# Kernel tuning notes

Measured on AMD Instinct MI355X. Metric: run time of the kernel, lower is better.

Reference implementation:

```python
import jax, jax.numpy as jnp
import numpy as np

D = 1024
H = 16
HD = D // H  # 64
HIDDEN = ((int(D * 8 / 3) + 63) // 64) * 64  # 2752
EPS = 1e-6


def rmsnorm(x, w):
    rms = jnp.sqrt(jnp.mean(x * x, axis=-1, keepdims=True) + EPS)
    return x / rms * w


def setup_inputs() -> dict:
    key = jax.random.key(0)
    ks = jax.random.split(key, 12)
    s = lambda fan_in: 1.0 / np.sqrt(fan_in)
    return {
        "x": jax.random.normal(ks[0], (4, 16, 256, D), dtype=jnp.float32),
        "time_emb": jax.random.normal(ks[1], (4, D), dtype=jnp.float32),
        "norm1_w": jnp.ones((D,), dtype=jnp.float32),
        "norm2_w": jnp.ones((D,), dtype=jnp.float32),
        # weights stored (in, out), i.e. transpose of torch nn.Linear.weight
        "qkv_w": jax.random.normal(ks[2], (D, 3 * H * HD), dtype=jnp.float32) * s(D),
        "out_w": jax.random.normal(ks[3], (H * HD, D), dtype=jnp.float32) * s(H * HD),
        "w1": jax.random.normal(ks[4], (D, HIDDEN), dtype=jnp.float32) * s(D),
        "w2": jax.random.normal(ks[5], (D, HIDDEN), dtype=jnp.float32) * s(D),
        "w3": jax.random.normal(ks[6], (HIDDEN, D), dtype=jnp.float32) * s(HIDDEN),
        "mod_w": jax.random.normal(ks[7], (D, 6 * D), dtype=jnp.float32) * s(D),
        "mod_b": jnp.zeros((6 * D,), dtype=jnp.float32),
    }


def spatial_attention(h, qkv_w, out_w):
    # h: (B, T, S, D); attention over S independently per (B, T)
    B, T, S, _ = h.shape
    qkv = jnp.einsum('btsd,de->btse', h, qkv_w)  # (B,T,S,3*H*HD)
    qkv = qkv.reshape(B, T, S, 3, H, HD)
    q, k, v = qkv[..., 0, :, :], qkv[..., 1, :, :], qkv[..., 2, :, :]  # (B,T,S,H,HD)
    scale = HD ** -0.5
    scores = jnp.einsum('btqhd,btkhd->bthqk', q, k) * scale  # (B,T,H,S,S)
    attn = jax.nn.softmax(scores, axis=-1)
    out = jnp.einsum('bthqk,btkhd->btqhd', attn, v).reshape(B, T, S, H * HD)
    return jnp.einsum('btse,ed->btsd', out, out_w)


def reference(x, time_emb, norm1_w, norm2_w, qkv_w, out_w, w1, w2, w3, mod_w, mod_b):
    # adaLN modulation from (B, D) time_emb -> broadcast over (T, S)
    mod = jax.nn.silu(time_emb) @ mod_w + mod_b  # (B, 6D)
    mod = mod[:, None, None, :]  # (B,1,1,6D)
    shift1, scale1, gate1, shift2, scale2, gate2 = jnp.split(mod, 6, axis=-1)

    h = rmsnorm(x, norm1_w) * (1.0 + scale1) + shift1
    h = spatial_attention(h, qkv_w, out_w)
    x = x + gate1 * h

    h = rmsnorm(x, norm2_w) * (1.0 + scale2) + shift2
    h = (jax.nn.silu(h @ w1) * (h @ w2)) @ w3  # SwiGLU
    x = x + gate2 * h
    return x
```

## Files before the change

kernel.cpp:

```cpp
#include <hip/hip_runtime.h>
#include <stdint.h>


using bf16x8 = __attribute__((ext_vector_type(8))) short;
using f32x4  = __attribute__((ext_vector_type(4))) float;

typedef __attribute__((address_space(3))) uint16_t lds16_t;

__device__ __forceinline__ float bf2f(uint16_t h) {
  union { uint32_t u; float f; } v; v.u = ((uint32_t)h) << 16; return v.f;
}
__device__ __forceinline__ uint16_t f2bf(float f) {
  union { float f; uint32_t u; } v; v.f = f;
  uint32_t r = v.u + 0x7FFFu + ((v.u >> 16) & 1u);
  return (uint16_t)(r >> 16);
}
__device__ __forceinline__ float silu(float x) { return x / (1.0f + __expf(-x)); }

__device__ __forceinline__ void gload16(const uint16_t* g, lds16_t* l) {
  __builtin_amdgcn_global_load_lds(
      (const __attribute__((address_space(1))) void*)g,
      (__attribute__((address_space(3))) void*)l, 16, 0, 0);
}

__device__ __forceinline__ bf16x8 lds_rd_b128(const uint16_t* p) {
  bf16x8 r;
  uint32_t a = (uint32_t)(uintptr_t)(const lds16_t*)p;
  asm volatile("ds_read_b128 %0, %1" : "=v"(r) : "v"(a) : "memory");
  return r;
}

__global__ __launch_bounds__(256)
void transpose_cast(const float* __restrict__ w, uint16_t* __restrict__ wt,
                    int K, int N, int ldt) {
  __shared__ float tile[32][33];
  int n0 = blockIdx.x * 32, k0 = blockIdx.y * 32;
  int tx = threadIdx.x & 31, ty = threadIdx.x >> 5;
#pragma unroll
  for (int it = 0; it < 4; ++it) {
    int r = ty + it * 8;
    tile[r][tx] = w[(size_t)(k0 + r) * N + n0 + tx];
  }
  __syncthreads();
#pragma unroll
  for (int it = 0; it < 4; ++it) {
    int r = ty + it * 8;
    wt[(size_t)(n0 + r) * ldt + k0 + tx] = f2bf(tile[tx][r]);
  }
}

__global__ __launch_bounds__(1024)
void mod_kernel(const float* __restrict__ te, const float* __restrict__ mw,
                const float* __restrict__ mb, float* __restrict__ mod) {
  __shared__ float ste[4096];
  __shared__ float red[4][4][256];
  int tid = threadIdx.x;
  for (int i = tid; i < 4096; i += 1024) { float v = te[i]; ste[i] = silu(v); }
  __syncthreads();
  int kslice = tid >> 8, cl = tid & 255;
  int col = blockIdx.x * 256 + cl;
  float acc[4] = {0.f, 0.f, 0.f, 0.f};
  for (int kk = 0; kk < 256; ++kk) {
    int k = kslice * 256 + kk;
    float wv = mw[k * 6144 + col];
#pragma unroll
    for (int b = 0; b < 4; ++b) acc[b] += ste[b * 1024 + k] * wv;
  }
#pragma unroll
  for (int b = 0; b < 4; ++b) red[kslice][b][cl] = acc[b];
  __syncthreads();
  if (kslice == 0) {
#pragma unroll
    for (int b = 0; b < 4; ++b)
      mod[b * 6144 + col] =
          red[0][b][cl] + red[1][b][cl] + red[2][b][cl] + red[3][b][cl] + mb[col];
  }
}

__global__ __launch_bounds__(256)
void norm_kernel(const float* __restrict__ xf,
                 const float* __restrict__ w, const float* __restrict__ mod,
                 int shift_off, int scale_off, uint16_t* __restrict__ out) {
  int row = blockIdx.x;
  int b = row >> 12;
  int tid = threadIdx.x;
  float4 t = *(const float4*)(xf + (size_t)row * 1024 + tid * 4);
  float v[4] = {t.x, t.y, t.z, t.w};
  float ss = v[0] * v[0] + v[1] * v[1] + v[2] * v[2] + v[3] * v[3];
#pragma unroll
  for (int off = 1; off < 64; off <<= 1) ss += __shfl_xor(ss, off);
  __shared__ float red[4];
  if ((tid & 63) == 0) red[tid >> 6] = ss;
  __syncthreads();
  float tot = red[0] + red[1] + red[2] + red[3];
  float rinv = rsqrtf(tot * (1.0f / 1024.0f) + 1e-6f);
  const float* mrow = mod + b * 6144;
  uint16_t o[4];
#pragma unroll
  for (int c = 0; c < 4; ++c) {
    int col = tid * 4 + c;
    float hv = v[c] * rinv * w[col] * (1.0f + mrow[scale_off + col]) + mrow[shift_off + col];
    o[c] = f2bf(hv);
  }
  uint2 pk;
  pk.x = (uint32_t)o[0] | ((uint32_t)o[1] << 16);
  pk.y = (uint32_t)o[2] | ((uint32_t)o[3] << 16);
  *(uint2*)(out + (size_t)row * 1024 + tid * 4) = pk;
}

#define BAR __builtin_amdgcn_s_barrier()
#define LGKM0                                            \
  do {                                                   \
    asm volatile("s_waitcnt lgkmcnt(0)" ::: "memory");   \
    __builtin_amdgcn_sched_barrier(0);                   \
  } while (0)
#define VMW(N) asm volatile("s_waitcnt vmcnt(" #N ")" ::: "memory")

#define GRD4(DST, BASE, ROWB, SWZ)                                           \
  {                                                                          \
    _Pragma("unroll") for (int q_ = 0; q_ < 4; ++q_)                         \
        DST[q_] = lds_rd_b128((BASE) + ((ROWB) + q_ * 16 + col) * 64 +       \
                              (SWZ));                                        \
  }

#define MM16(I0, AF)                                                         \
  {                                                                          \
    __builtin_amdgcn_s_setprio(1);                                           \
    _Pragma("unroll") for (int q_ = 0; q_ < 4; ++q_) {                       \
      _Pragma("unroll") for (int j_ = 0; j_ < 4; ++j_)                       \
          acc[(I0) + q_][j_] = __builtin_amdgcn_mfma_f32_16x16x32_bf16(      \
              AF[q_], bf[j_], acc[(I0) + q_][j_], 0, 0, 0);                  \
    }                                                                        \
    __builtin_amdgcn_s_setprio(0);                                           \
  }

#define ADST(S, H, G) ((lds16_t*)As[(S)] + (H) * 8192 + (G) * 4096 + sdoff)
#define BDST(S, H, G) ((lds16_t*)Bs[(S)] + (H) * 8192 + (G) * 4096 + sdoff)

#define TILE(S, KA, KB, DO_A, DO_B, VMTAIL)                                  \
  {                                                                          \
    bf16x8 af[4], bf[4];                                                     \
                                                                \
    GRD4(af, As[S], wm * 128, swz0);                                         \
    GRD4(bf, Bs[S], wn * 64, swz0);                                          \
    if (DO_A) {                                                              \
      gload16(aS00 + (KA), ADST((S) ^ 1, 0, 0));                             \
      gload16(aS01 + (KA), ADST((S) ^ 1, 0, 1));                             \
    }                                                                        \
    BAR; LGKM0;                                                              \
    MM16(0, af);                                                             \
    BAR;                                                                     \
                                                                \
    GRD4(af, As[S], wm * 128 + 64, swz0);                                    \
    if (DO_A) {                                                              \
      gload16(aS10 + (KA), ADST((S) ^ 1, 1, 0));                             \
      gload16(aS11 + (KA), ADST((S) ^ 1, 1, 1));                             \
    }                                                                        \
    BAR; LGKM0;                                                              \
    MM16(4, af);                                                             \
    BAR;                                                                     \
                                                                \
    GRD4(af, As[S], wm * 128, swz1);                                         \
    GRD4(bf, Bs[S], wn * 64, swz1);                                          \
    BAR; LGKM0;                                                              \
    MM16(0, af);                                                             \
    BAR;                                                                     \
                                                                \
    GRD4(af, As[S], wm * 128 + 64, swz1);                                    \
    if (DO_B) {                                                              \
      gload16(bS00 + (KB), BDST(S, 0, 0));                                   \
      gload16(bS01 + (KB), BDST(S, 0, 1));                                   \
      gload16(bS10 + (KB), BDST(S, 1, 0));                                   \
      gload16(bS11 + (KB), BDST(S, 1, 1));                                   \
    }                                                                        \
    BAR; LGKM0;                                                              \
    MM16(4, af);                                                             \
    VMTAIL;                                                                  \
    BAR;                                                                     \
  }

template <int MODE>
__global__ __launch_bounds__(512)
void gemm256(const uint16_t* __restrict__ A, int lda,
             const uint16_t* __restrict__ Bt, int ldb,
             int N, int K, int ldc,
             uint16_t* __restrict__ obf, const float* __restrict__ xin,
             const float* __restrict__ mod, const uint16_t* __restrict__ h1,
             float* __restrict__ xio) {
  __shared__ uint16_t As[2][16384];
  __shared__ uint16_t Bs[2][16384];
  const int tiles_n = N >> 8;
  const int xcd = blockIdx.x & 7;
  const int bslot = blockIdx.x >> 3;
  const int tm = (bslot / tiles_n) * 8 + xcd;
  const int tn = bslot % tiles_n;
  const int m0 = tm * 256, n0 = tn * 256;
  const int tid = threadIdx.x;
  const int wave = tid >> 6, lane = tid & 63;
  const int wm = wave >> 2, wn = wave & 3;
  const int col = lane & 15, quad = lane >> 4;
  const int c7 = col & 7;
  const int swz0 = (quad ^ c7) << 3;
  const int swz1 = ((4 + quad) ^ c7) << 3;
  const int sdoff = wave * 512 + lane * 8;

  const int srl = lane >> 3;
  const int sl8 = ((lane & 7) ^ srl) << 3;
  const int rg0 = wave * 8 + srl;
  const int rg1 = 64 + wave * 8 + srl;
  const uint16_t* aS00 = A + (size_t)(m0 + rg0) * lda + sl8;
  const uint16_t* aS01 = A + (size_t)(m0 + rg1) * lda + sl8;
  const uint16_t* aS10 = A + (size_t)(m0 + 128 + rg0) * lda + sl8;
  const uint16_t* aS11 = A + (size_t)(m0 + 128 + rg1) * lda + sl8;
  const uint16_t* bS00 = Bt + (size_t)(n0 + rg0) * ldb + sl8;
  const uint16_t* bS01 = Bt + (size_t)(n0 + rg1) * ldb + sl8;
  const uint16_t* bS10 = Bt + (size_t)(n0 + 128 + rg0) * ldb + sl8;
  const uint16_t* bS11 = Bt + (size_t)(n0 + 128 + rg1) * ldb + sl8;

  f32x4 acc[8][4];
#pragma unroll
  for (int i = 0; i < 8; ++i)
#pragma unroll
    for (int j = 0; j < 4; ++j) acc[i][j] = (f32x4){0.f, 0.f, 0.f, 0.f};

  gload16(bS00, BDST(0, 0, 0)); gload16(bS01, BDST(0, 0, 1));
  gload16(bS10, BDST(0, 1, 0)); gload16(bS11, BDST(0, 1, 1));
  gload16(aS00, ADST(0, 0, 0)); gload16(aS01, ADST(0, 0, 1));
  gload16(aS10, ADST(0, 1, 0)); gload16(aS11, ADST(0, 1, 1));
  gload16(bS00 + 64, BDST(1, 0, 0)); gload16(bS01 + 64, BDST(1, 0, 1));
  gload16(bS10 + 64, BDST(1, 1, 0)); gload16(bS11 + 64, BDST(1, 1, 1));
  VMW(4);
  BAR;

  const int NT = K >> 6;
  int k0 = 0;
  for (int t = 0; t + 2 < NT; t += 2) {
    TILE(0, k0 + 64, k0 + 128, true, true, VMW(4));
    TILE(1, k0 + 128, k0 + 192, true, true, VMW(4));
    k0 += 128;
  }
  TILE(0, k0 + 64, 0, true, false, VMW(0));
  TILE(1, 0, 0, false, false, (void)0);

  __builtin_amdgcn_sched_barrier(0);

#pragma unroll
  for (int i = 0; i < 8; ++i) {
#pragma unroll
    for (int j = 0; j < 4; ++j) {
#pragma unroll
      for (int r = 0; r < 4; ++r) {
        int row = m0 + wm * 128 + i * 16 + quad * 4 + r;
        int cn = n0 + wn * 64 + j * 16 + col;
        float c = acc[i][j][r];
        if (MODE == 0) {
          obf[(size_t)row * ldc + cn] = f2bf(c);
        } else if (MODE == 1) {
          int b = row >> 12;
          size_t idx = (size_t)row * 1024 + cn;
          float g = mod[b * 6144 + 2048 + cn];
          xio[idx] = xin[idx] + g * c;
        } else {
          int b = row >> 12;
          size_t idx = (size_t)row * 1024 + cn;
          float g = mod[b * 6144 + 5120 + cn];
          xio[idx] = xio[idx] + g * c;
        }
      }
    }
  }
}

#define MMF(ACC, AF, BF)                                                     \
  {                                                                          \
    __builtin_amdgcn_s_setprio(1);                                           \
    _Pragma("unroll") for (int i_ = 0; i_ < 4; ++i_) {                       \
      _Pragma("unroll") for (int j_ = 0; j_ < 4; ++j_)                       \
          ACC[i_][j_] = __builtin_amdgcn_mfma_f32_16x16x32_bf16(             \
              AF[i_], BF[j_], ACC[i_][j_], 0, 0, 0);                         \
    }                                                                        \
    __builtin_amdgcn_s_setprio(0);                                           \
  }

#define FAD(S, H)  ((lds16_t*)As[(S)]  + (H) * 4096 + sdoff)
#define FB1D(S, H) ((lds16_t*)B1s[(S)] + (H) * 4096 + sdoff)
#define FB2D(S, H) ((lds16_t*)B2s[(S)] + (H) * 4096 + sdoff)

#define FTILE(S, KN, KB, DO_AB2, DO_B1, VMTAIL)                              \
  {                                                                          \
    bf16x8 af[4], bb[4];                                                     \
                      \
    GRD4(af, As[S], wm * 64, swz0);                                          \
    GRD4(bb, B1s[S], wn * 64, swz0);                                         \
    if (DO_AB2) {                                                            \
      gload16(aS[0] + (KN), FAD((S) ^ 1, 0));                                \
      gload16(aS[1] + (KN), FAD((S) ^ 1, 1));                                \
      gload16(b2S[0] + (KN), FB2D((S) ^ 1, 0));                              \
      gload16(b2S[1] + (KN), FB2D((S) ^ 1, 1));                              \
    }                                                                        \
    BAR; LGKM0;                                                              \
    MMF(acc1, af, bb);                                                       \
    BAR;                                                                     \
                                        \
    GRD4(bb, B2s[S], wn * 64, swz0);                                         \
    if (DO_AB2) {                                                            \
      gload16(aS[2] + (KN), FAD((S) ^ 1, 2));                                \
      gload16(aS[3] + (KN), FAD((S) ^ 1, 3));                                \
    }                                                                        \
    BAR; LGKM0;                                                              \
    MMF(acc2, af, bb);                                                       \
    BAR;                                                                     \
                                                     \
    GRD4(af, As[S], wm * 64, swz1);                                          \
    GRD4(bb, B1s[S], wn * 64, swz1);                                         \
    BAR; LGKM0;                                                              \
    MMF(acc1, af, bb);                                                       \
    BAR;                                                                     \
                                             \
    GRD4(bb, B2s[S], wn * 64, swz1);                                         \
    if (DO_B1) {                                                             \
      gload16(b1S[0] + (KB), FB1D(S, 0));                                    \
      gload16(b1S[1] + (KB), FB1D(S, 1));                                    \
    }                                                                        \
    BAR; LGKM0;                                                              \
    MMF(acc2, af, bb);                                                       \
    VMTAIL;                                                                  \
    BAR;                                                                     \
  }

__global__ __launch_bounds__(512)
void gemm_ffn(const uint16_t* __restrict__ A, const uint16_t* __restrict__ B1t,
              const uint16_t* __restrict__ B2t, uint16_t* __restrict__ outp) {
  __shared__ uint16_t As[2][16384];
  __shared__ uint16_t B1s[2][8192];
  __shared__ uint16_t B2s[2][8192];
  const int lda = 1024, ldb = 1024, ldc = 2816;
  const int tiles_n = 22;
  const int xcd = blockIdx.x & 7;
  const int bslot = blockIdx.x >> 3;
  const int tm = (bslot / tiles_n) * 8 + xcd;
  const int tn = bslot % tiles_n;
  const int m0 = tm * 256, n0 = tn * 128;
  const int tid = threadIdx.x;
  const int wave = tid >> 6, lane = tid & 63;
  const int wm = wave >> 1, wn = wave & 1;
  const int col = lane & 15, quad = lane >> 4;
  const int c7 = col & 7;
  const int swz0 = (quad ^ c7) << 3;
  const int swz1 = ((4 + quad) ^ c7) << 3;
  const int sdoff = wave * 512 + lane * 8;
  const int srl = lane >> 3;
  const int sl8 = ((lane & 7) ^ srl) << 3;
  const int rg = wave * 8 + srl;

  const uint16_t* aS[4];
#pragma unroll
  for (int h = 0; h < 4; ++h)
    aS[h] = A + (size_t)(m0 + h * 64 + rg) * lda + sl8;
  const uint16_t* b1S[2]; const uint16_t* b2S[2];
#pragma unroll
  for (int h = 0; h < 2; ++h) {
    b1S[h] = B1t + (size_t)(n0 + h * 64 + rg) * ldb + sl8;
    b2S[h] = B2t + (size_t)(n0 + h * 64 + rg) * ldb + sl8;
  }

  f32x4 acc1[4][4], acc2[4][4];
#pragma unroll
  for (int i = 0; i < 4; ++i)
#pragma unroll
    for (int j = 0; j < 4; ++j) {
      acc1[i][j] = (f32x4){0.f, 0.f, 0.f, 0.f};
      acc2[i][j] = (f32x4){0.f, 0.f, 0.f, 0.f};
    }

#pragma unroll
  for (int h = 0; h < 4; ++h) gload16(aS[h], FAD(0, h));
  gload16(b1S[0], FB1D(0, 0)); gload16(b1S[1], FB1D(0, 1));
  gload16(b2S[0], FB2D(0, 0)); gload16(b2S[1], FB2D(0, 1));
  gload16(b1S[0] + 64, FB1D(1, 0)); gload16(b1S[1] + 64, FB1D(1, 1));
  VMW(2);
  BAR;

  int k0 = 0;
  for (int t = 0; t + 2 < 16; t += 2) {
    FTILE(0, k0 + 64, k0 + 128, true, true, VMW(2));
    FTILE(1, k0 + 128, k0 + 192, true, true, VMW(2));
    k0 += 128;
  }
  FTILE(0, k0 + 64, 0, true, false, VMW(0));
  FTILE(1, 0, 0, false, false, (void)0);

  __builtin_amdgcn_sched_barrier(0);

#pragma unroll
  for (int i = 0; i < 4; ++i) {
#pragma unroll
    for (int j = 0; j < 4; ++j) {
#pragma unroll
      for (int r = 0; r < 4; ++r) {
        int row = m0 + wm * 64 + i * 16 + quad * 4 + r;
        int cn = n0 + wn * 64 + j * 16 + col;
        float c1 = acc1[i][j][r];
        float c2 = acc2[i][j][r];
        outp[(size_t)row * ldc + cn] = f2bf(silu(c1) * c2);
      }
    }
  }
}

__global__ __launch_bounds__(256)
void attn_kernel(const uint16_t* __restrict__ qkv, uint16_t* __restrict__ out) {
  __shared__ uint16_t lds[32768];
  const int tid = threadIdx.x;
  const int bid = blockIdx.x;
  const int slice = bid >> 2, qc = bid & 3;
  const int bt = slice >> 4, h = slice & 15;
  const int row0 = bt * 256;
  const int wave = tid >> 6, lane = tid & 63;
  const int col = lane & 15, quad = lane >> 4;

  {
    int kr = tid;
    const uint16_t* kp = qkv + (size_t)(row0 + kr) * 3072 + 1024 + h * 64;
    uint16_t* ks = lds + kr * 64;
#pragma unroll
    for (int kc = 0; kc < 8; ++kc) {
      uint4 v = *(const uint4*)(kp + kc * 8);
      *(uint4*)(ks + ((kc ^ (kr & 7)) << 3)) = v;
    }
  }
  {
    int p = tid & 127, dh = tid >> 7;
    const uint16_t* vp0 = qkv + (size_t)(row0 + 2 * p) * 3072 + 2048 + h * 64 + dh * 32;
    const uint16_t* vp1 = vp0 + 3072;
    uint16_t r0[32], r1[32];
#pragma unroll
    for (int i = 0; i < 4; ++i) {
      *(uint4*)(r0 + i * 8) = *(const uint4*)(vp0 + i * 8);
      *(uint4*)(r1 + i * 8) = *(const uint4*)(vp1 + i * 8);
    }
    uint32_t* vt = (uint32_t*)(lds + 16384);
    int krc = p >> 2;
#pragma unroll
    for (int i = 0; i < 32; ++i) {
      int d = dh * 32 + i;
      uint32_t val = (uint32_t)r0[i] | ((uint32_t)r1[i] << 16);
      vt[d * 128 + ((krc ^ (d & 7)) << 2) + (p & 3)] = val;
    }
  }
  __syncthreads();

  const int qrow = qc * 64 + wave * 16 + col;
  const uint16_t* qp = qkv + (size_t)(row0 + qrow) * 3072 + h * 64;
  bf16x8 aq0 = *(const bf16x8*)(qp + quad * 8);
  bf16x8 aq1 = *(const bf16x8*)(qp + 32 + quad * 8);

  f32x4 sc[16];
#pragma unroll
  for (int t = 0; t < 16; ++t) {
    int n = t * 16 + col;
    const uint16_t* kb = lds + n * 64;
    bf16x8 b0 = *(const bf16x8*)(kb + ((quad ^ (n & 7)) << 3));
    bf16x8 b1 = *(const bf16x8*)(kb + (((4 + quad) ^ (n & 7)) << 3));
    f32x4 s = (f32x4){0.f, 0.f, 0.f, 0.f};
    s = __builtin_amdgcn_mfma_f32_16x16x32_bf16(aq0, b0, s, 0, 0, 0);
    s = __builtin_amdgcn_mfma_f32_16x16x32_bf16(aq1, b1, s, 0, 0, 0);
    sc[t] = s;
  }

  const float scale = 0.125f;
  float inv[4];
#pragma unroll
  for (int i = 0; i < 4; ++i) {
    float m = -1e30f;
#pragma unroll
    for (int t = 0; t < 16; ++t) m = fmaxf(m, sc[t][i]);
    m = fmaxf(m, __shfl_xor(m, 1));
    m = fmaxf(m, __shfl_xor(m, 2));
    m = fmaxf(m, __shfl_xor(m, 4));
    m = fmaxf(m, __shfl_xor(m, 8));
    m *= scale;
    float sum = 0.f;
#pragma unroll
    for (int t = 0; t < 16; ++t) {
      float p = __expf(sc[t][i] * scale - m);
      sc[t][i] = p;
      sum += p;
    }
    sum += __shfl_xor(sum, 1);
    sum += __shfl_xor(sum, 2);
    sum += __shfl_xor(sum, 4);
    sum += __shfl_xor(sum, 8);
    inv[i] = 1.0f / sum;
  }
  __syncthreads();

  uint16_t* P = lds + wave * 4096;
#pragma unroll
  for (int t = 0; t < 16; ++t) {
    int pcb = t * 2 + (col >> 3);
#pragma unroll
    for (int i = 0; i < 4; ++i) {
      int r = quad * 4 + i;
      P[r * 256 + ((pcb ^ (r & 7)) << 3) + (col & 7)] = f2bf(sc[t][i] * inv[i]);
    }
  }

  f32x4 o[4];
#pragma unroll
  for (int nt = 0; nt < 4; ++nt) o[nt] = (f32x4){0.f, 0.f, 0.f, 0.f};
  const uint16_t* Vt = lds + 16384;
#pragma unroll
  for (int c = 0; c < 8; ++c) {
    int pc = c * 4 + quad;
    bf16x8 ap = *(const bf16x8*)(P + col * 256 + ((pc ^ (col & 7)) << 3));
#pragma unroll
    for (int nt = 0; nt < 4; ++nt) {
      int d = nt * 16 + col;
      bf16x8 bv = *(const bf16x8*)(Vt + d * 256 + ((pc ^ (d & 7)) << 3));
      o[nt] = __builtin_amdgcn_mfma_f32_16x16x32_bf16(ap, bv, o[nt], 0, 0, 0);
    }
  }

#pragma unroll
  for (int nt = 0; nt < 4; ++nt) {
#pragma unroll
    for (int r = 0; r < 4; ++r) {
      int grow = row0 + qc * 64 + wave * 16 + quad * 4 + r;
      int gcol = h * 64 + nt * 16 + col;
      out[(size_t)grow * 1024 + gcol] = f2bf(o[nt][r]);
    }
  }
}

extern "C" void kernel_launch(void* const* d_in, const int* in_sizes, int n_in,
                              void* d_out, int out_size, void* d_ws, size_t ws_size,
                              hipStream_t stream) {
  const float* x        = (const float*)d_in[0];
  const float* time_emb = (const float*)d_in[1];
  const float* norm1_w  = (const float*)d_in[2];
  const float* norm2_w  = (const float*)d_in[3];
  const float* qkv_w    = (const float*)d_in[4];
  const float* out_w    = (const float*)d_in[5];
  const float* w1       = (const float*)d_in[6];
  const float* w2       = (const float*)d_in[7];
  const float* w3       = (const float*)d_in[8];
  const float* mod_w    = (const float*)d_in[9];
  const float* mod_b    = (const float*)d_in[10];
  float* out = (float*)d_out;

  char* ws = (char*)d_ws;
  float*    mod    = (float*)(ws);
  uint16_t* wqkv_t = (uint16_t*)(ws + 98304);
  uint16_t* wout_t = (uint16_t*)(ws + 6389760);
  uint16_t* w1t    = (uint16_t*)(ws + 8486912);
  uint16_t* w2t    = (uint16_t*)(ws + 14254080);
  uint16_t* w3t    = (uint16_t*)(ws + 20021248);
  uint16_t* hbuf   = (uint16_t*)(ws + 25788416);
  uint16_t* qkvb   = (uint16_t*)(ws + 59342848);
  uint16_t* hid    = qkvb;

  hipMemsetAsync(w1t, 0, (size_t)2816 * 1024 * 2, stream);
  hipMemsetAsync(w2t, 0, (size_t)2816 * 1024 * 2, stream);
  hipMemsetAsync(w3t, 0, (size_t)1024 * 2816 * 2, stream);

  dim3 blk(256);
  transpose_cast<<<dim3(96, 32), blk, 0, stream>>>(qkv_w, wqkv_t, 1024, 3072, 1024);
  transpose_cast<<<dim3(32, 32), blk, 0, stream>>>(out_w, wout_t, 1024, 1024, 1024);
  transpose_cast<<<dim3(86, 32), blk, 0, stream>>>(w1, w1t, 1024, 2752, 1024);
  transpose_cast<<<dim3(86, 32), blk, 0, stream>>>(w2, w2t, 1024, 2752, 1024);
  transpose_cast<<<dim3(32, 86), blk, 0, stream>>>(w3, w3t, 2752, 1024, 2816);

  mod_kernel<<<24, 1024, 0, stream>>>(time_emb, mod_w, mod_b, mod);

  norm_kernel<<<16384, blk, 0, stream>>>(x, norm1_w, mod, 0, 1024, hbuf);

  gemm256<0><<<768, 512, 0, stream>>>(hbuf, 1024, wqkv_t, 1024, 3072, 1024, 3072,
                                      qkvb, nullptr, nullptr, nullptr, nullptr);
  attn_kernel<<<4096, blk, 0, stream>>>(qkvb, hbuf);

  gemm256<1><<<256, 512, 0, stream>>>(hbuf, 1024, wout_t, 1024, 1024, 1024, 1024,
                                      nullptr, x, mod, nullptr, out);
  norm_kernel<<<16384, blk, 0, stream>>>(out, norm2_w, mod, 3072, 4096, hbuf);

  gemm_ffn<<<1408, 512, 0, stream>>>(hbuf, w1t, w2t, hid);

  gemm256<4><<<256, 512, 0, stream>>>(hid, 2816, w3t, 2816, 1024, 2816, 1024,
                                      nullptr, nullptr, mod, nullptr, out);
}
```

Measured before the change: 757.6 us.

## Make FFN GEMM persistent over N tiles with cross-tile prefetch

```diff
diff --git a/kernel.cpp b/kernel.cpp
--- a/kernel.cpp
+++ b/kernel.cpp
@@ -286,17 +286,18 @@
 #define FB1D(S, H) ((lds16_t*)B1s[(S)] + (H) * 4096 + sdoff)
 #define FB2D(S, H) ((lds16_t*)B2s[(S)] + (H) * 4096 + sdoff)
 
-#define FTILE(S, KN, KB, DO_AB2, DO_B1, VMTAIL)                              \
+#define FTILE(S, PA0, PA1, PA2, PA3, PB2A, PB2B, PB1A, PB1B, DO_AB2, DO_B1,  \
+              VMTAIL)                                                        \
   {                                                                          \
     bf16x8 af[4], bb[4];                                                     \
                       \
     GRD4(af, As[S], wm * 64, swz0);                                          \
     GRD4(bb, B1s[S], wn * 64, swz0);                                         \
     if (DO_AB2) {                                                            \
-      gload16(aS[0] + (KN), FAD((S) ^ 1, 0));                                \
-      gload16(aS[1] + (KN), FAD((S) ^ 1, 1));                                \
-      gload16(b2S[0] + (KN), FB2D((S) ^ 1, 0));                              \
-      gload16(b2S[1] + (KN), FB2D((S) ^ 1, 1));                              \
+      gload16((PA0), FAD((S) ^ 1, 0));                                       \
+      gload16((PA1), FAD((S) ^ 1, 1));                                       \
+      gload16((PB2A), FB2D((S) ^ 1, 0));                                     \
+      gload16((PB2B), FB2D((S) ^ 1, 1));                                     \
     }                                                                        \
     BAR; LGKM0;                                                              \
     MMF(acc1, af, bb);                                                       \
@@ -304,8 +305,8 @@
                                         \
     GRD4(bb, B2s[S], wn * 64, swz0);                                         \
     if (DO_AB2) {                                                            \
-      gload16(aS[2] + (KN), FAD((S) ^ 1, 2));                                \
-      gload16(aS[3] + (KN), FAD((S) ^ 1, 3));                                \
+      gload16((PA2), FAD((S) ^ 1, 2));                                       \
+      gload16((PA3), FAD((S) ^ 1, 3));                                       \
     }                                                                        \
     BAR; LGKM0;                                                              \
     MMF(acc2, af, bb);                                                       \
@@ -319,8 +320,8 @@
                                              \
     GRD4(bb, B2s[S], wn * 64, swz1);                                         \
     if (DO_B1) {                                                             \
-      gload16(b1S[0] + (KB), FB1D(S, 0));                                    \
-      gload16(b1S[1] + (KB), FB1D(S, 1));                                    \
+      gload16((PB1A), FB1D(S, 0));                                           \
+      gload16((PB1B), FB1D(S, 1));                                           \
     }                                                                        \
     BAR; LGKM0;                                                              \
     MMF(acc2, af, bb);                                                       \
@@ -335,12 +336,12 @@
   __shared__ uint16_t B1s[2][8192];
   __shared__ uint16_t B2s[2][8192];
   const int lda = 1024, ldb = 1024, ldc = 2816;
-  const int tiles_n = 22;
-  const int xcd = blockIdx.x & 7;
-  const int bslot = blockIdx.x >> 3;
-  const int tm = (bslot / tiles_n) * 8 + xcd;
-  const int tn = bslot % tiles_n;
-  const int m0 = tm * 256, n0 = tn * 128;
+  const int bid = blockIdx.x;
+  const int tm = bid & 63;
+  const int g = bid >> 6;
+  const int tn0 = (g < 2) ? g * 6 : 12 + (g - 2) * 5;
+  const int J   = (g < 2) ? 6 : 5;
+  const int m0 = tm * 256;
   const int tid = threadIdx.x;
   const int wave = tid >> 6, lane = tid & 63;
   const int wm = wave >> 1, wn = wave & 1;
@@ -357,12 +358,12 @@
 #pragma unroll
   for (int h = 0; h < 4; ++h)
     aS[h] = A + (size_t)(m0 + h * 64 + rg) * lda + sl8;
-  const uint16_t* b1S[2]; const uint16_t* b2S[2];
-#pragma unroll
-  for (int h = 0; h < 2; ++h) {
-    b1S[h] = B1t + (size_t)(n0 + h * 64 + rg) * ldb + sl8;
-    b2S[h] = B2t + (size_t)(n0 + h * 64 + rg) * ldb + sl8;
-  }
+
+  const size_t BSTEP = (size_t)128 * 1024;
+  const uint16_t* b1c0 = B1t + (size_t)(tn0 * 128 + rg) * ldb + sl8;
+  const uint16_t* b1c1 = b1c0 + (size_t)64 * ldb;
+  const uint16_t* b2c0 = B2t + (size_t)(tn0 * 128 + rg) * ldb + sl8;
+  const uint16_t* b2c1 = b2c0 + (size_t)64 * ldb;
 
   f32x4 acc1[4][4], acc2[4][4];
 #pragma unroll
@@ -375,36 +376,65 @@
 
 #pragma unroll
   for (int h = 0; h < 4; ++h) gload16(aS[h], FAD(0, h));
-  gload16(b1S[0], FB1D(0, 0)); gload16(b1S[1], FB1D(0, 1));
-  gload16(b2S[0], FB2D(0, 0)); gload16(b2S[1], FB2D(0, 1));
-  gload16(b1S[0] + 64, FB1D(1, 0)); gload16(b1S[1] + 64, FB1D(1, 1));
+  gload16(b1c0, FB1D(0, 0)); gload16(b1c1, FB1D(0, 1));
+  gload16(b2c0, FB2D(0, 0)); gload16(b2c1, FB2D(0, 1));
+  gload16(b1c0 + 64, FB1D(1, 0)); gload16(b1c1 + 64, FB1D(1, 1));
   VMW(2);
   BAR;
 
-  int k0 = 0;
-  for (int t = 0; t + 2 < 16; t += 2) {
-    FTILE(0, k0 + 64, k0 + 128, true, true, VMW(2));
-    FTILE(1, k0 + 128, k0 + 192, true, true, VMW(2));
-    k0 += 128;
-  }
-  FTILE(0, k0 + 64, 0, true, false, VMW(0));
-  FTILE(1, 0, 0, false, false, (void)0);
-
-  __builtin_amdgcn_sched_barrier(0);
-
-#pragma unroll
-  for (int i = 0; i < 4; ++i) {
-#pragma unroll
-    for (int j = 0; j < 4; ++j) {
-#pragma unroll
-      for (int r = 0; r < 4; ++r) {
-        int row = m0 + wm * 64 + i * 16 + quad * 4 + r;
-        int cn = n0 + wn * 64 + j * 16 + col;
-        float c1 = acc1[i][j][r];
-        float c2 = acc2[i][j][r];
-        outp[(size_t)row * ldc + cn] = f2bf(silu(c1) * c2);
+#pragma unroll 1
+  for (int jb = 0; jb < J; ++jb) {
+    const bool lst = (jb == J - 1);
+    const uint16_t* b1n0 = b1c0 + BSTEP;
+    const uint16_t* b1n1 = b1c1 + BSTEP;
+    const uint16_t* b2n0 = b2c0 + BSTEP;
+    const uint16_t* b2n1 = b2c1 + BSTEP;
+
+    int k0 = 0;
+#pragma unroll 1
+    for (int p = 0; p < 7; ++p) {
+      FTILE(0, aS[0] + k0 + 64, aS[1] + k0 + 64, aS[2] + k0 + 64,
+            aS[3] + k0 + 64, b2c0 + k0 + 64, b2c1 + k0 + 64,
+            b1c0 + k0 + 128, b1c1 + k0 + 128, true, true, VMW(2));
+      FTILE(1, aS[0] + k0 + 128, aS[1] + k0 + 128, aS[2] + k0 + 128,
+            aS[3] + k0 + 128, b2c0 + k0 + 128, b2c1 + k0 + 128,
+            b1c0 + k0 + 192, b1c1 + k0 + 192, true, true, VMW(2));
+      k0 += 128;
+    }
+    if (!lst) {
+      FTILE(0, aS[0] + 960, aS[1] + 960, aS[2] + 960, aS[3] + 960,
+            b2c0 + 960, b2c1 + 960, b1n0, b1n1, true, true, VMW(2));
+      FTILE(1, aS[0], aS[1], aS[2], aS[3], b2n0, b2n1,
+            b1n0 + 64, b1n1 + 64, true, true, VMW(2));
+    } else {
+      FTILE(0, aS[0] + 960, aS[1] + 960, aS[2] + 960, aS[3] + 960,
+            b2c0 + 960, b2c1 + 960, b1c0, b1c1, true, false, VMW(0));
+      FTILE(1, aS[0], aS[1], aS[2], aS[3], b2c0, b2c1, b1c0, b1c1,
+            false, false, (void)0);
+    }
+
+    __builtin_amdgcn_sched_barrier(0);
+
+    const int n0j = (tn0 + jb) * 128;
+#pragma unroll
+    for (int i = 0; i < 4; ++i) {
+#pragma unroll
+      for (int jj = 0; jj < 4; ++jj) {
+#pragma unroll
+        for (int r = 0; r < 4; ++r) {
+          int row = m0 + wm * 64 + i * 16 + quad * 4 + r;
+          int cn = n0j + wn * 64 + jj * 16 + col;
+          float c1 = acc1[i][jj][r];
+          float c2 = acc2[i][jj][r];
+          outp[(size_t)row * ldc + cn] = f2bf(silu(c1) * c2);
+          acc1[i][jj][r] = 0.f;
+          acc2[i][jj][r] = 0.f;
+        }
       }
     }
+    __builtin_amdgcn_sched_barrier(0);
+
+    b1c0 = b1n0; b1c1 = b1n1; b2c0 = b2n0; b2c1 = b2n1;
   }
 }
 
@@ -583,7 +613,7 @@
                                       nullptr, x, mod, nullptr, out);
   norm_kernel<<<16384, blk, 0, stream>>>(out, norm2_w, mod, 3072, 4096, hbuf);
 
-  gemm_ffn<<<1408, 512, 0, stream>>>(hbuf, w1t, w2t, hid);
+  gemm_ffn<<<256, 512, 0, stream>>>(hbuf, w1t, w2t, hid);
 
   gemm256<4><<<256, 512, 0, stream>>>(hid, 2816, w3t, 2816, 1024, 2816, 1024,
                                       nullptr, nullptr, mod, nullptr, out);
```

Measured after the change: 1.099 ms. +45.1%, slower.
